# Kernel tuning notes

Hardware: AMD Instinct MI355X
Metric: run time of the kernel (lower is better)

Reference implementation:

```python
import math
import jax, jax.numpy as jnp
import numpy as np
from jax import lax

# Block_mamba(dim=192): x = x + Mamba(LN1(x)); x = x + EinFFT(LN2(x), H, W)
DIM = 192
D_STATE = 64
D_CONV = 4
EXPAND = 2
D_INNER = EXPAND * DIM          # 384
DT_RANK = math.ceil(DIM / 16)   # 12
NUM_BLOCKS = 4                  # EinFFT hardcoded
BLOCK_SIZE = DIM // NUM_BLOCKS  # 48
LAMBDA = 0.01                   # softshrink threshold


def setup_inputs() -> dict:
    key = jax.random.key(0)
    ks = jax.random.split(key, 20)
    B, N, C = 4, 1024, DIM
    s = 0.02
    x = jax.random.normal(ks[0], (B, N, C), jnp.float32)
    inp = {
        "x": x,
        "ln1_w": jnp.ones((C,), jnp.float32),
        "ln1_b": jnp.zeros((C,), jnp.float32),
        "in_proj_w": jax.random.normal(ks[1], (2 * D_INNER, C), jnp.float32) * s,
        "conv_w": jax.random.normal(ks[2], (D_INNER, 1, D_CONV), jnp.float32) * 0.1,
        "conv_b": jnp.zeros((D_INNER,), jnp.float32),
        "x_proj_w": jax.random.normal(ks[3], (DT_RANK + 2 * D_STATE, D_INNER), jnp.float32) * s,
        "dt_proj_w": jax.random.normal(ks[4], (D_INNER, DT_RANK), jnp.float32) * (DT_RANK ** -0.5),
        "dt_proj_b": jax.random.uniform(ks[5], (D_INNER,), jnp.float32, -4.0, -2.0),
        "A_log": jnp.log(jnp.broadcast_to(jnp.arange(1, D_STATE + 1, dtype=jnp.float32), (D_INNER, D_STATE))),
        "D": jnp.ones((D_INNER,), jnp.float32),
        "out_proj_w": jax.random.normal(ks[6], (C, D_INNER), jnp.float32) * s,
        "ln2_w": jnp.ones((C,), jnp.float32),
        "ln2_b": jnp.zeros((C,), jnp.float32),
        "cw1": jax.random.normal(ks[7], (2, NUM_BLOCKS, BLOCK_SIZE, BLOCK_SIZE), jnp.float32) * s,
        "cw2": jax.random.normal(ks[8], (2, NUM_BLOCKS, BLOCK_SIZE, BLOCK_SIZE), jnp.float32) * s,
        "cb1": jax.random.normal(ks[9], (2, NUM_BLOCKS, BLOCK_SIZE), jnp.float32) * s,
        "cb2": jax.random.normal(ks[10], (2, NUM_BLOCKS, BLOCK_SIZE), jnp.float32) * s,
        "H": 32,
        "W": 32,
    }
    return inp


def layer_norm(x, w, b, eps=1e-5):
    mu = jnp.mean(x, axis=-1, keepdims=True)
    var = jnp.var(x, axis=-1, keepdims=True)
    return (x - mu) * lax.rsqrt(var + eps) * w + b


def mamba(x, in_proj_w, conv_w, conv_b, x_proj_w, dt_proj_w, dt_proj_b, A_log, D):
    B, L, C = x.shape
    xz = jnp.einsum('blc,ec->ble', x, in_proj_w)          # [B,L,2*D_INNER]
    xm, z = jnp.split(xz, 2, axis=-1)                      # each [B,L,D_INNER]
    # causal depthwise conv1d (torch pads both sides then slices [:, :, :L])
    xc = lax.conv_general_dilated(
        xm.transpose(0, 2, 1), conv_w, (1,), [(D_CONV - 1, 0)],
        dimension_numbers=('NCH', 'OIH', 'NCH'), feature_group_count=D_INNER)
    xm = jax.nn.silu(xc + conv_b[None, :, None]).transpose(0, 2, 1)  # [B,L,D_INNER]
    dbc = jnp.einsum('bld,ed->ble', xm, x_proj_w)
    dt, Bm, Cm = jnp.split(dbc, [DT_RANK, DT_RANK + D_STATE], axis=-1)
    delta = jax.nn.softplus(jnp.einsum('blr,dr->bld', dt, dt_proj_w) + dt_proj_b)  # [B,L,D_INNER]
    A = -jnp.exp(A_log)                                    # [D_INNER, D_STATE]

    def step(h, inp):
        d_t, B_t, C_t, x_t = inp                           # [B,d],[B,n],[B,n],[B,d]
        dA = jnp.exp(d_t[:, :, None] * A)                  # [B,d,n]
        h = h * dA + (d_t * x_t)[:, :, None] * B_t[:, None, :]
        y = jnp.einsum('bdn,bn->bd', h, C_t)
        return h, y

    h0 = jnp.zeros((B, D_INNER, D_STATE), x.dtype)
    xs = (delta.transpose(1, 0, 2), Bm.transpose(1, 0, 2), Cm.transpose(1, 0, 2), xm.transpose(1, 0, 2))
    _, ys = lax.scan(step, h0, xs)                         # ys: [L,B,d]
    y = ys.transpose(1, 0, 2) + xm * D
    y = y * jax.nn.silu(z)
    return jnp.einsum('bld,cd->blc', y, out_proj_w_global[0])


# small trick to keep mamba signature tidy
out_proj_w_global = [None]


def einfft(x, cw1, cw2, cb1, cb2):
    B, N, C = x.shape
    xv = x.reshape(B, N, NUM_BLOCKS, BLOCK_SIZE)
    pad1 = (1 << math.ceil(math.log2(N))) - N
    pad2 = (1 << math.ceil(math.log2(NUM_BLOCKS))) - NUM_BLOCKS
    if pad1 or pad2:
        xv = jnp.pad(xv, ((0, 0), (0, pad1), (0, pad2), (0, 0)))
    X = jnp.fft.fft2(xv, axes=(1, 2), norm='ortho')
    mul = lambda t, w: jnp.einsum('Bnbd,bdk->Bnbk', t, w)
    r1 = jax.nn.relu(mul(X.real, cw1[0]) - mul(X.imag, cw1[1]) + cb1[0])
    i1 = jax.nn.relu(mul(X.real, cw1[1]) + mul(X.imag, cw1[0]) + cb1[1])
    r2 = mul(r1, cw2[0]) - mul(i1, cw2[1]) + cb2[0]
    i2 = mul(r1, cw2[1]) + mul(i1, cw2[0]) + cb2[1]
    ss = lambda v: jnp.where(v > LAMBDA, v - LAMBDA, jnp.where(v < -LAMBDA, v + LAMBDA, jnp.zeros((), v.dtype)))
    Z = ss(r2) + 1j * ss(i2)
    y = jnp.fft.ifft2(Z, axes=(1, 2), norm='ortho')[:, :N, :NUM_BLOCKS, :]
    return y.real.reshape(B, N, C)  # torch .to(real dtype) keeps real part


def reference(x, ln1_w, ln1_b, in_proj_w, conv_w, conv_b, x_proj_w, dt_proj_w, dt_proj_b,
              A_log, D, out_proj_w, ln2_w, ln2_b, cw1, cw2, cb1, cb2, H, W):
    out_proj_w_global[0] = out_proj_w
    x = x + mamba(layer_norm(x, ln1_w, ln1_b), in_proj_w, conv_w, conv_b,
                  x_proj_w, dt_proj_w, dt_proj_b, A_log, D)
    x = x + einfft(layer_norm(x, ln2_w, ln2_b), cw1, cw2, cb1, cb2)
    return x
```

## Files before the change

### kernel.cpp

```cpp
#include <hip/hip_runtime.h>
#include <math.h>

#define PI_F 3.14159265358979323846f

__device__ __forceinline__ float lane_bcast(float v, int l) {
  return __int_as_float(__builtin_amdgcn_readlane(__float_as_int(v), l));
}

__device__ __forceinline__ float wave_reduce_sum(float v) {
  v += __shfl_xor(v, 32, 64);
  v += __shfl_xor(v, 16, 64);
  v += __shfl_xor(v, 8, 64);
  v += __shfl_xor(v, 4, 64);
  v += __shfl_xor(v, 2, 64);
  v += __shfl_xor(v, 1, 64);
  return v;
}

__global__ __launch_bounds__(256) void ln_kernel(const float* __restrict__ x,
    const float* __restrict__ w, const float* __restrict__ b, float* __restrict__ o) {
  int row = blockIdx.x * 4 + (threadIdx.x >> 6);
  int lane = threadIdx.x & 63;
  const float* xr = x + (size_t)row * 192;
  float v0 = xr[lane], v1 = xr[lane + 64], v2 = xr[lane + 128];
  float s  = wave_reduce_sum(v0 + v1 + v2);
  float s2 = wave_reduce_sum(v0 * v0 + v1 * v1 + v2 * v2);
  float mu  = s * (1.f / 192.f);
  float var = s2 * (1.f / 192.f) - mu * mu;
  float rs  = rsqrtf(var + 1e-5f);
  float* orow = o + (size_t)row * 192;
  orow[lane]       = (v0 - mu) * rs * w[lane]       + b[lane];
  orow[lane + 64]  = (v1 - mu) * rs * w[lane + 64]  + b[lane + 64];
  orow[lane + 128] = (v2 - mu) * rs * w[lane + 128] + b[lane + 128];
}

__global__ __launch_bounds__(256) void ln2t_kernel(const float* __restrict__ x,
    const float* __restrict__ w, const float* __restrict__ b, float* __restrict__ xT) {
  __shared__ float xt[32][193];
  __shared__ float mu_s[32], rs_s[32];
  int blk = blockIdx.x;
  int Bi = blk >> 5;
  int t0 = (blk & 31) * 32;
  int tid = threadIdx.x;
  const float* xb = x + ((size_t)(Bi * 1024 + t0)) * 192;
  for (int i = tid; i < 32 * 192; i += 256) {
    xt[i / 192][i % 192] = xb[i];
  }
  __syncthreads();
  int row = tid >> 3, seg = tid & 7;
  float s = 0.f, s2 = 0.f;
  const float* xr = &xt[row][seg * 24];
#pragma unroll
  for (int k = 0; k < 24; ++k) { float v = xr[k]; s += v; s2 += v * v; }
  s  += __shfl_xor(s, 1, 64);  s  += __shfl_xor(s, 2, 64);  s  += __shfl_xor(s, 4, 64);
  s2 += __shfl_xor(s2, 1, 64); s2 += __shfl_xor(s2, 2, 64); s2 += __shfl_xor(s2, 4, 64);
  if (seg == 0) {
    float mu = s * (1.f / 192.f);
    float var = s2 * (1.f / 192.f) - mu * mu;
    mu_s[row] = mu;
    rs_s[row] = rsqrtf(var + 1e-5f);
  }
  __syncthreads();
  for (int i = tid; i < 32 * 192; i += 256) {
    int ch = i >> 5, r2 = i & 31;
    float v = (xt[r2][ch] - mu_s[r2]) * rs_s[r2] * w[ch] + b[ch];
    xT[((size_t)(Bi * 192 + ch)) * 1024 + t0 + r2] = v;
  }
}

__global__ __launch_bounds__(256) void gemm_tn(const float* __restrict__ A,
    const float* __restrict__ W, const float* __restrict__ res, float* __restrict__ C,
    int M, int N, int K) {
  __shared__ float As[2][32][68];
  __shared__ float Ws[2][32][68];
  int tid = threadIdx.x;
  int m0 = blockIdx.y * 64, n0 = blockIdx.x * 64;
  int tr = tid >> 4, tc = tid & 15;
  int sm  = tid >> 3;
  int skq = tid & 7;
  float4 aP[2], wP[2];
#pragma unroll
  for (int j = 0; j < 2; ++j) {
    int m = sm + j * 32;
    aP[j] = *(const float4*)(A + (size_t)(m0 + m) * K + skq * 4);
    int n = n0 + m;
    if (n < N) wP[j] = *(const float4*)(W + (size_t)n * K + skq * 4);
    else       wP[j] = make_float4(0.f, 0.f, 0.f, 0.f);
  }
#pragma unroll
  for (int j = 0; j < 2; ++j) {
    int m = sm + j * 32;
    As[0][skq * 4 + 0][m] = aP[j].x;
    As[0][skq * 4 + 1][m] = aP[j].y;
    As[0][skq * 4 + 2][m] = aP[j].z;
    As[0][skq * 4 + 3][m] = aP[j].w;
    Ws[0][skq * 4 + 0][m] = wP[j].x;
    Ws[0][skq * 4 + 1][m] = wP[j].y;
    Ws[0][skq * 4 + 2][m] = wP[j].z;
    Ws[0][skq * 4 + 3][m] = wP[j].w;
  }
  __syncthreads();
  float acc[4][4] = {{0.f}};
  int nk = K >> 5;
  for (int it = 0; it < nk; ++it) {
    int cur = it & 1, nxt = cur ^ 1;
    if (it + 1 < nk) {
      int kk = (it + 1) << 5;
#pragma unroll
      for (int j = 0; j < 2; ++j) {
        int m = sm + j * 32;
        aP[j] = *(const float4*)(A + (size_t)(m0 + m) * K + kk + skq * 4);
        int n = n0 + m;
        if (n < N) wP[j] = *(const float4*)(W + (size_t)n * K + kk + skq * 4);
        else       wP[j] = make_float4(0.f, 0.f, 0.f, 0.f);
      }
    }
#pragma unroll
    for (int k = 0; k < 32; ++k) {
      float4 a4 = *(const float4*)&As[cur][k][tr * 4];
      float4 w4 = *(const float4*)&Ws[cur][k][tc * 4];
      float a[4] = {a4.x, a4.y, a4.z, a4.w};
      float bb[4] = {w4.x, w4.y, w4.z, w4.w};
#pragma unroll
      for (int i = 0; i < 4; ++i)
#pragma unroll
        for (int j = 0; j < 4; ++j)
          acc[i][j] = fmaf(a[i], bb[j], acc[i][j]);
    }
    if (it + 1 < nk) {
#pragma unroll
      for (int j = 0; j < 2; ++j) {
        int m = sm + j * 32;
        As[nxt][skq * 4 + 0][m] = aP[j].x;
        As[nxt][skq * 4 + 1][m] = aP[j].y;
        As[nxt][skq * 4 + 2][m] = aP[j].z;
        As[nxt][skq * 4 + 3][m] = aP[j].w;
        Ws[nxt][skq * 4 + 0][m] = wP[j].x;
        Ws[nxt][skq * 4 + 1][m] = wP[j].y;
        Ws[nxt][skq * 4 + 2][m] = wP[j].z;
        Ws[nxt][skq * 4 + 3][m] = wP[j].w;
      }
      __syncthreads();
    }
  }
#pragma unroll
  for (int i = 0; i < 4; ++i) {
    int m = m0 + tr * 4 + i;
#pragma unroll
    for (int j = 0; j < 4; ++j) {
      int n = n0 + tc * 4 + j;
      if (n < N) {
        float v = acc[i][j];
        if (res) v += res[m * N + n];
        C[m * N + n] = v;
      }
    }
  }
}

__global__ __launch_bounds__(256) void gemm_tn32(const float* __restrict__ A,
    const float* __restrict__ W, const float* __restrict__ res, float* __restrict__ C,
    int M, int N, int K) {
  __shared__ float As[2][32][36];
  __shared__ float Ws[2][32][68];
  int tid = threadIdx.x;
  int m0 = blockIdx.y * 32, n0 = blockIdx.x * 64;
  int tr = tid >> 4, tc = tid & 15;
  int sm  = tid >> 3;
  int skq = tid & 7;
  float4 aP, wP[2];
  aP = *(const float4*)(A + (size_t)(m0 + sm) * K + skq * 4);
#pragma unroll
  for (int j = 0; j < 2; ++j) {
    int n = n0 + sm + j * 32;
    if (n < N) wP[j] = *(const float4*)(W + (size_t)n * K + skq * 4);
    else       wP[j] = make_float4(0.f, 0.f, 0.f, 0.f);
  }
  As[0][skq * 4 + 0][sm] = aP.x;
  As[0][skq * 4 + 1][sm] = aP.y;
  As[0][skq * 4 + 2][sm] = aP.z;
  As[0][skq * 4 + 3][sm] = aP.w;
#pragma unroll
  for (int j = 0; j < 2; ++j) {
    int n = sm + j * 32;
    Ws[0][skq * 4 + 0][n] = wP[j].x;
    Ws[0][skq * 4 + 1][n] = wP[j].y;
    Ws[0][skq * 4 + 2][n] = wP[j].z;
    Ws[0][skq * 4 + 3][n] = wP[j].w;
  }
  __syncthreads();
  float acc[2][4] = {{0.f}};
  int nk = K >> 5;
  for (int it = 0; it < nk; ++it) {
    int cur = it & 1, nxt = cur ^ 1;
    if (it + 1 < nk) {
      int kk = (it + 1) << 5;
      aP = *(const float4*)(A + (size_t)(m0 + sm) * K + kk + skq * 4);
#pragma unroll
      for (int j = 0; j < 2; ++j) {
        int n = n0 + sm + j * 32;
        if (n < N) wP[j] = *(const float4*)(W + (size_t)n * K + kk + skq * 4);
        else       wP[j] = make_float4(0.f, 0.f, 0.f, 0.f);
      }
    }
#pragma unroll
    for (int k = 0; k < 32; ++k) {
      float2 a2 = *(const float2*)&As[cur][k][tr * 2];
      float4 w4 = *(const float4*)&Ws[cur][k][tc * 4];
      float a[2] = {a2.x, a2.y};
      float bb[4] = {w4.x, w4.y, w4.z, w4.w};
#pragma unroll
      for (int i = 0; i < 2; ++i)
#pragma unroll
        for (int j = 0; j < 4; ++j)
          acc[i][j] = fmaf(a[i], bb[j], acc[i][j]);
    }
    if (it + 1 < nk) {
      As[nxt][skq * 4 + 0][sm] = aP.x;
      As[nxt][skq * 4 + 1][sm] = aP.y;
      As[nxt][skq * 4 + 2][sm] = aP.z;
      As[nxt][skq * 4 + 3][sm] = aP.w;
#pragma unroll
      for (int j = 0; j < 2; ++j) {
        int n = sm + j * 32;
        Ws[nxt][skq * 4 + 0][n] = wP[j].x;
        Ws[nxt][skq * 4 + 1][n] = wP[j].y;
        Ws[nxt][skq * 4 + 2][n] = wP[j].z;
        Ws[nxt][skq * 4 + 3][n] = wP[j].w;
      }
      __syncthreads();
    }
  }
#pragma unroll
  for (int i = 0; i < 2; ++i) {
    int m = m0 + tr * 2 + i;
#pragma unroll
    for (int j = 0; j < 4; ++j) {
      int n = n0 + tc * 4 + j;
      if (n < N) {
        float v = acc[i][j];
        if (res) v += res[m * N + n];
        C[m * N + n] = v;
      }
    }
  }
}

__global__ __launch_bounds__(256) void gemm_at32(const float* __restrict__ AT,
    const float* __restrict__ W, const float* __restrict__ res, float* __restrict__ C,
    int M, int N, int K) {
  __shared__ float As[2][32][36];
  __shared__ float Ws[2][32][68];
  int tid = threadIdx.x;
  int m0 = blockIdx.y * 32, n0 = blockIdx.x * 64;
  int bb = m0 >> 10;
  int t0 = m0 & 1023;
  const float* Ab = AT + ((size_t)bb * K) * 1024 + t0;
  int tr = tid >> 4, tc = tid & 15;
  int sm  = tid >> 3;
  int skq = tid & 7;
  float4 aP, wP[2];
  aP = *(const float4*)(Ab + (size_t)sm * 1024 + skq * 4);
#pragma unroll
  for (int j = 0; j < 2; ++j) {
    int n = n0 + sm + j * 32;
    if (n < N) wP[j] = *(const float4*)(W + (size_t)n * K + skq * 4);
    else       wP[j] = make_float4(0.f, 0.f, 0.f, 0.f);
  }
  *(float4*)&As[0][sm][skq * 4] = aP;
#pragma unroll
  for (int j = 0; j < 2; ++j) {
    int n = sm + j * 32;
    Ws[0][skq * 4 + 0][n] = wP[j].x;
    Ws[0][skq * 4 + 1][n] = wP[j].y;
    Ws[0][skq * 4 + 2][n] = wP[j].z;
    Ws[0][skq * 4 + 3][n] = wP[j].w;
  }
  __syncthreads();
  float acc[2][4] = {{0.f}};
  int nk = K >> 5;
  for (int it = 0; it < nk; ++it) {
    int cur = it & 1, nxt = cur ^ 1;
    if (it + 1 < nk) {
      int kk = (it + 1) << 5;
      aP = *(const float4*)(Ab + (size_t)(kk + sm) * 1024 + skq * 4);
#pragma unroll
      for (int j = 0; j < 2; ++j) {
        int n = n0 + sm + j * 32;
        if (n < N) wP[j] = *(const float4*)(W + (size_t)n * K + kk + skq * 4);
        else       wP[j] = make_float4(0.f, 0.f, 0.f, 0.f);
      }
    }
#pragma unroll
    for (int k = 0; k < 32; ++k) {
      float2 a2 = *(const float2*)&As[cur][k][tr * 2];
      float4 w4 = *(const float4*)&Ws[cur][k][tc * 4];
      float a[2] = {a2.x, a2.y};
      float bb4[4] = {w4.x, w4.y, w4.z, w4.w};
#pragma unroll
      for (int i = 0; i < 2; ++i)
#pragma unroll
        for (int j = 0; j < 4; ++j)
          acc[i][j] = fmaf(a[i], bb4[j], acc[i][j]);
    }
    if (it + 1 < nk) {
      *(float4*)&As[nxt][sm][skq * 4] = aP;
#pragma unroll
      for (int j = 0; j < 2; ++j) {
        int n = sm + j * 32;
        Ws[nxt][skq * 4 + 0][n] = wP[j].x;
        Ws[nxt][skq * 4 + 1][n] = wP[j].y;
        Ws[nxt][skq * 4 + 2][n] = wP[j].z;
        Ws[nxt][skq * 4 + 3][n] = wP[j].w;
      }
      __syncthreads();
    }
  }
#pragma unroll
  for (int i = 0; i < 2; ++i) {
    int m = m0 + tr * 2 + i;
#pragma unroll
    for (int j = 0; j < 4; ++j) {
      int n = n0 + tc * 4 + j;
      if (n < N) {
        float v = acc[i][j];
        if (res) v += res[m * N + n];
        C[m * N + n] = v;
      }
    }
  }
}

__global__ __launch_bounds__(256) void conv_silu(const float* __restrict__ xz,
    const float* __restrict__ cw, const float* __restrict__ cb, float* __restrict__ xc) {
  int e4 = blockIdx.x * 256 + threadIdx.x;
  if (e4 >= 4 * 1024 * 96) return;
  int d4 = e4 % 96;
  int t  = (e4 / 96) % 1024;
  int b  = e4 / (96 * 1024);
  int d = d4 * 4;
  const float* base = xz + (size_t)(b * 1024) * 768 + d;
  float4 acc = *(const float4*)(cb + d);
  const float4* cwv = (const float4*)(cw + d * 4);
  float4 c0 = cwv[0], c1 = cwv[1], c2 = cwv[2], c3 = cwv[3];
#pragma unroll
  for (int j = 0; j < 4; ++j) {
    int tt = t - 3 + j;
    if (tt >= 0) {
      float4 v = *(const float4*)(base + (size_t)tt * 768);
      float w0 = (&c0.x)[j], w1 = (&c1.x)[j], w2 = (&c2.x)[j], w3 = (&c3.x)[j];
      acc.x = fmaf(v.x, w0, acc.x);
      acc.y = fmaf(v.y, w1, acc.y);
      acc.z = fmaf(v.z, w2, acc.z);
      acc.w = fmaf(v.w, w3, acc.w);
    }
  }
  float4 o;
  o.x = acc.x / (1.f + __expf(-acc.x));
  o.y = acc.y / (1.f + __expf(-acc.y));
  o.z = acc.z / (1.f + __expf(-acc.z));
  o.w = acc.w / (1.f + __expf(-acc.w));
  *(float4*)(xc + ((size_t)(b * 1024 + t) * 384) + d) = o;
}

__global__ __launch_bounds__(256) void delta_trans(const float* __restrict__ dbc,
    const float* __restrict__ dtw, const float* __restrict__ dtb,
    const float* __restrict__ xc, float* __restrict__ dltT, float* __restrict__ duT) {
  __shared__ float dts[64][13];
  __shared__ float xt[64][65];
  int blk = blockIdx.x;
  int b  = blk / 96;
  int rem = blk % 96;
  int tt = rem / 6, dd = rem % 6;
  int t0 = tt * 64, d0 = dd * 64;
  int tid = threadIdx.x;
  for (int i = tid; i < 64 * 12; i += 256) {
    int tl = i / 12, r = i % 12;
    dts[tl][r] = dbc[((size_t)b * 1024 + t0 + tl) * 140 + r];
  }
  {
    int col = tid & 63, rg = tid >> 6;
#pragma unroll
    for (int j = 0; j < 16; ++j) {
      int row = j * 4 + rg;
      xt[row][col] = xc[((size_t)b * 1024 + t0 + row) * 384 + d0 + col];
    }
  }
  __syncthreads();
  int tl = tid & 63, grp = tid >> 6;
#pragma unroll
  for (int j = 0; j < 16; ++j) {
    int dl = grp * 16 + j;
    int d = d0 + dl;
    float s = dtb[d];
#pragma unroll
    for (int r = 0; r < 12; ++r) s += dts[tl][r] * dtw[d * 12 + r];
    float dlt = (s > 20.f) ? s : log1pf(__expf(s));
    size_t ob = ((size_t)b * 384 + d) * 1024 + t0 + tl;
    dltT[ob] = dlt;
    duT[ob]  = dlt * xt[tl][dl];
  }
}

__global__ __launch_bounds__(128) void scan_pc(const float* __restrict__ dltT,
    const float* __restrict__ duT, const float* __restrict__ dbc,
    const float* __restrict__ A_log, const float* __restrict__ xc,
    const float* __restrict__ xz, const float* __restrict__ Dvec,
    float* __restrict__ yT) {
  __shared__ float Bs[2][16][64];
  __shared__ float Cs[2][16][64];
  __shared__ float dvs[2][64], dus[2][64];
  __shared__ float xcs[2][16], zvs[2][16];
  __shared__ float tile[16][65];
  int bd = blockIdx.x;
  int b = bd / 384, d = bd % 384;
  int tid = threadIdx.x;
  int wv = tid >> 6;
  int lane = tid & 63;
  const float* dT = dltT + ((size_t)b * 384 + d) * 1024;
  const float* uT = duT  + ((size_t)b * 384 + d) * 1024;
  const float* Bbase = dbc + (size_t)(b * 1024) * 140 + 12;
  const float* xcp = xc + (size_t)(b * 1024) * 384 + d;
  const float* xzp = xz + (size_t)(b * 1024) * 768 + 384 + d;
  float* yp = yT + ((size_t)b * 384 + d) * 1024;

  float A = 0.f, ddv = 0.f;
  int tq = lane & 15, q = lane >> 4;
  if (wv == 1) {
#pragma unroll
    for (int i = 0; i < 16; ++i) {
      size_t ro = (size_t)i * 140 + lane;
      Bs[0][i][lane] = Bbase[ro];
      Cs[0][i][lane] = Bbase[ro + 64];
    }
    dvs[0][lane] = dT[lane];
    dus[0][lane] = uT[lane];
    if (lane < 16) {
      xcs[0][lane] = xcp[(size_t)lane * 384];
      zvs[0][lane] = xzp[(size_t)lane * 768];
    }
  } else {
    A = -__expf(A_log[d * 64 + lane]) * 1.44269504f;
    ddv = Dvec[d];
  }
  __syncthreads();

  float h = 0.f, dv64 = 0.f, du64 = 0.f;
  for (int g = 0; g < 64; ++g) {
    int cur = g & 1, nxt = cur ^ 1;
    if (wv == 1) {
      if (g < 63) {
        int ts1 = (g + 1) * 16;
#pragma unroll
        for (int i = 0; i < 16; ++i) {
          size_t ro = (size_t)(ts1 + i) * 140 + lane;
          Bs[nxt][i][lane] = Bbase[ro];
          Cs[nxt][i][lane] = Bbase[ro + 64];
        }
        if (lane < 16) {
          xcs[nxt][lane] = xcp[(size_t)(ts1 + lane) * 384];
          zvs[nxt][lane] = xzp[(size_t)(ts1 + lane) * 768];
        }
        if (((g + 1) & 3) == 0) {
          int sseg = (g + 1) >> 2;
          int sl = sseg & 1;
          dvs[sl][lane] = dT[sseg * 64 + lane];
          dus[sl][lane] = uT[sseg * 64 + lane];
        }
      }
    } else {
      if ((g & 3) == 0) {
        int sl = (g >> 2) & 1;
        dv64 = dvs[sl][lane];
        du64 = dus[sl][lane];
      }
      int ts = g * 16, tb = ts & 63;
      float Bv[16], Cv[16];
#pragma unroll
      for (int i = 0; i < 16; ++i) {
        Bv[i] = Bs[cur][i][lane];
        Cv[i] = Cs[cur][i][lane];
      }
      float xcv = 0.f, zv = 0.f;
      if (lane < 16) { xcv = xcs[cur][lane]; zv = zvs[cur][lane]; }
#pragma unroll
      for (int i = 0; i < 16; ++i) {
        float sdv = lane_bcast(dv64, tb + i);
        float sdu = lane_bcast(du64, tb + i);
        float a = exp2f(sdv * A);
        h = fmaf(h, a, sdu * Bv[i]);
        tile[i][lane] = h * Cv[i];
      }
      const float* trow = &tile[tq][q * 16];
      float s_ = 0.f;
#pragma unroll
      for (int i = 0; i < 16; ++i) s_ += trow[i];
      s_ += __shfl_xor(s_, 16, 64);
      s_ += __shfl_xor(s_, 32, 64);
      if (lane < 16) {
        float sg = zv / (1.f + __expf(-zv));
        yp[ts + lane] = (s_ + xcv * ddv) * sg;
      }
    }
    __syncthreads();
  }
}

__device__ __forceinline__ int rev4_10(int i) {
  unsigned r = __brev((unsigned)i) >> 22;
  return (int)(((r & 0x155u) << 1) | ((r >> 1) & 0x155u));
}

__device__ __forceinline__ void fft1024r4(float* __restrict__ re,
    float* __restrict__ im, const float* __restrict__ twc,
    const float* __restrict__ tws, int tid, float sgn) {
  for (int i = tid; i < 1024; i += 256) {
    int r = rev4_10(i);
    if (i < r) {
      float t = re[i]; re[i] = re[r]; re[r] = t;
      t = im[i]; im[i] = im[r]; im[r] = t;
    }
  }
  __syncthreads();
  {
    float4 ar = *(float4*)&re[tid * 4];
    float4 ai = *(float4*)&im[tid * 4];
    float apc_r = ar.x + ar.z, amc_r = ar.x - ar.z;
    float apc_i = ai.x + ai.z, amc_i = ai.x - ai.z;
    float bpd_r = ar.y + ar.w, bmd_r = ar.y - ar.w;
    float bpd_i = ai.y + ai.w, bmd_i = ai.y - ai.w;
    float4 yr, yi;
    yr.x = apc_r + bpd_r;        yi.x = apc_i + bpd_i;
    yr.z = apc_r - bpd_r;        yi.z = apc_i - bpd_i;
    yr.y = amc_r - sgn * bmd_i;  yi.y = amc_i + sgn * bmd_r;
    yr.w = amc_r + sgn * bmd_i;  yi.w = amc_i - sgn * bmd_r;
    *(float4*)&re[tid * 4] = yr;
    *(float4*)&im[tid * 4] = yi;
  }
  __syncthreads();
#pragma unroll
  for (int s = 1; s < 5; ++s) {
    int L = 1 << (2 * s);
    int tstep = 256 >> (2 * s);
    int j = tid & (L - 1);
    int base = ((tid >> (2 * s)) << (2 * s + 2)) + j;
    int i0 = base, i1 = base + L, i2 = base + 2 * L, i3 = base + 3 * L;
    int x1i = j * tstep;
    float w1c = twc[x1i],     w1s = tws[x1i];
    float w2c = twc[2 * x1i], w2s = tws[2 * x1i];
    float w3c = twc[3 * x1i], w3s = tws[3 * x1i];
    float ar_ = re[i0], ai_ = im[i0];
    float br_ = re[i1], bi_ = im[i1];
    float cr_ = re[i2], ci_ = im[i2];
    float dr_ = re[i3], di_ = im[i3];
    float tbr = br_ * w1c - bi_ * w1s, tbi = br_ * w1s + bi_ * w1c;
    float tcr = cr_ * w2c - ci_ * w2s, tci = cr_ * w2s + ci_ * w2c;
    float tdr = dr_ * w3c - di_ * w3s, tdi = dr_ * w3s + di_ * w3c;
    float apc_r = ar_ + tcr, amc_r = ar_ - tcr;
    float apc_i = ai_ + tci, amc_i = ai_ - tci;
    float bpd_r = tbr + tdr, bmd_r = tbr - tdr;
    float bpd_i = tbi + tdi, bmd_i = tbi - tdi;
    re[i0] = apc_r + bpd_r;       im[i0] = apc_i + bpd_i;
    re[i2] = apc_r - bpd_r;       im[i2] = apc_i - bpd_i;
    re[i1] = amc_r - sgn * bmd_i; im[i1] = amc_i + sgn * bmd_r;
    re[i3] = amc_r + sgn * bmd_i; im[i3] = amc_i - sgn * bmd_r;
    __syncthreads();
  }
}

__global__ __launch_bounds__(256) void fft_fwd(const float* __restrict__ x2T,
    float* __restrict__ Xre, float* __restrict__ Xim) {
  __shared__ float re[1024];
  __shared__ float im[1024];
  __shared__ float twc[768];
  __shared__ float tws[768];
  int blk = blockIdx.x;
  int c = blk & 3;
  int rest = blk >> 2;
  int d = rest % 48, Bi = rest / 48;
  int tid = threadIdx.x;
  for (int k = tid; k < 768; k += 256) {
    float sv, cv;
    __sincosf(-PI_F * (float)k * (1.f / 512.f), &sv, &cv);
    twc[k] = cv; tws[k] = sv;
  }
  const float* pb = x2T + ((size_t)(Bi * 192 + d)) * 1024;
  for (int n = tid; n < 1024; n += 256) {
    float v0 = pb[n];
    float v1 = pb[48 * 1024 + n];
    float v2 = pb[96 * 1024 + n];
    float v3 = pb[144 * 1024 + n];
    float rr, ii;
    if (c == 0)      { rr = v0 + v1 + v2 + v3; ii = 0.f; }
    else if (c == 1) { rr = v0 - v2;           ii = -(v1 - v3); }
    else if (c == 2) { rr = v0 - v1 + v2 - v3; ii = 0.f; }
    else             { rr = v0 - v2;           ii = (v1 - v3); }
    re[n] = rr; im[n] = ii;
  }
  __syncthreads();
  fft1024r4(re, im, twc, tws, tid, -1.0f);
  float* xo_r = Xre + ((size_t)((Bi * 4 + c) * 48 + d)) * 1024;
  float* xo_i = Xim + ((size_t)((Bi * 4 + c) * 48 + d)) * 1024;
  for (int k = tid; k < 1024; k += 256) {
    xo_r[k] = re[k] * (1.f / 64.f);
    xo_i[k] = im[k] * (1.f / 64.f);
  }
}

__global__ __launch_bounds__(256) void mix_fused(float* __restrict__ Xre,
    float* __restrict__ Xim, const float* __restrict__ cw1,
    const float* __restrict__ cw2, const float* __restrict__ cb1,
    const float* __restrict__ cb2) {
  __shared__ float r1s[4][48][4];
  __shared__ float i1s[4][48][4];
  int w = threadIdx.x >> 6;
  int j = threadIdx.x & 63;
  int rg = blockIdx.x * 4 + w;
  int kq = rg & 255;
  int b  = (rg >> 8) & 3;
  int Bi = rg >> 10;
  int k0 = kq * 4;
  size_t xbase = ((size_t)((Bi * 4 + b) * 48)) * 1024 + k0;
  if (j < 48) {
    const float* wr = cw1 + b * 2304;
    const float* wi = cw1 + 9216 + b * 2304;
    float b1r = cb1[b * 48 + j], b1i = cb1[192 + b * 48 + j];
    float ar[4] = {b1r, b1r, b1r, b1r};
    float ai[4] = {b1i, b1i, b1i, b1i};
#pragma unroll 8
    for (int dd = 0; dd < 48; ++dd) {
      float4 xr = *(const float4*)(Xre + xbase + (size_t)dd * 1024);
      float4 xi = *(const float4*)(Xim + xbase + (size_t)dd * 1024);
      float wrv = wr[dd * 48 + j], wiv = wi[dd * 48 + j];
      ar[0] = fmaf(xr.x, wrv, ar[0]); ar[0] = fmaf(-xi.x, wiv, ar[0]);
      ai[0] = fmaf(xr.x, wiv, ai[0]); ai[0] = fmaf(xi.x, wrv, ai[0]);
      ar[1] = fmaf(xr.y, wrv, ar[1]); ar[1] = fmaf(-xi.y, wiv, ar[1]);
      ai[1] = fmaf(xr.y, wiv, ai[1]); ai[1] = fmaf(xi.y, wrv, ai[1]);
      ar[2] = fmaf(xr.z, wrv, ar[2]); ar[2] = fmaf(-xi.z, wiv, ar[2]);
      ai[2] = fmaf(xr.z, wiv, ai[2]); ai[2] = fmaf(xi.z, wrv, ai[2]);
      ar[3] = fmaf(xr.w, wrv, ar[3]); ar[3] = fmaf(-xi.w, wiv, ar[3]);
      ai[3] = fmaf(xr.w, wiv, ai[3]); ai[3] = fmaf(xi.w, wrv, ai[3]);
    }
    float4 r1v, i1v;
    r1v.x = fmaxf(ar[0], 0.f); r1v.y = fmaxf(ar[1], 0.f);
    r1v.z = fmaxf(ar[2], 0.f); r1v.w = fmaxf(ar[3], 0.f);
    i1v.x = fmaxf(ai[0], 0.f); i1v.y = fmaxf(ai[1], 0.f);
    i1v.z = fmaxf(ai[2], 0.f); i1v.w = fmaxf(ai[3], 0.f);
    *(float4*)&r1s[w][j][0] = r1v;
    *(float4*)&i1s[w][j][0] = i1v;
    const float* wr2 = cw2 + b * 2304;
    const float* wi2 = cw2 + 9216 + b * 2304;
    float b2r = cb2[b * 48 + j], b2i = cb2[192 + b * 48 + j];
    float a2r[4] = {b2r, b2r, b2r, b2r};
    float a2i[4] = {b2i, b2i, b2i, b2i};
#pragma unroll 8
    for (int dd = 0; dd < 48; ++dd) {
      float4 rv = *(const float4*)&r1s[w][dd][0];
      float4 iv = *(const float4*)&i1s[w][dd][0];
      float wrv = wr2[dd * 48 + j], wiv = wi2[dd * 48 + j];
      a2r[0] = fmaf(rv.x, wrv, a2r[0]); a2r[0] = fmaf(-iv.x, wiv, a2r[0]);
      a2i[0] = fmaf(rv.x, wiv, a2i[0]); a2i[0] = fmaf(iv.x, wrv, a2i[0]);
      a2r[1] = fmaf(rv.y, wrv, a2r[1]); a2r[1] = fmaf(-iv.y, wiv, a2r[1]);
      a2i[1] = fmaf(rv.y, wiv, a2i[1]); a2i[1] = fmaf(iv.y, wrv, a2i[1]);
      a2r[2] = fmaf(rv.z, wrv, a2r[2]); a2r[2] = fmaf(-iv.z, wiv, a2r[2]);
      a2i[2] = fmaf(rv.z, wiv, a2i[2]); a2i[2] = fmaf(iv.z, wrv, a2i[2]);
      a2r[3] = fmaf(rv.w, wrv, a2r[3]); a2r[3] = fmaf(-iv.w, wiv, a2r[3]);
      a2i[3] = fmaf(rv.w, wiv, a2i[3]); a2i[3] = fmaf(iv.w, wrv, a2i[3]);
    }
    float4 zr, zi;
#pragma unroll
    for (int r = 0; r < 4; ++r) {
      float vr = a2r[r], vi = a2i[r];
      (&zr.x)[r] = (vr > 0.01f) ? vr - 0.01f : ((vr < -0.01f) ? vr + 0.01f : 0.f);
      (&zi.x)[r] = (vi > 0.01f) ? vi - 0.01f : ((vi < -0.01f) ? vi + 0.01f : 0.f);
    }
    size_t obase = ((size_t)((Bi * 4 + b) * 48 + j)) * 1024 + k0;
    *(float4*)(Xre + obase) = zr;
    *(float4*)(Xim + obase) = zi;
  }
}

__global__ __launch_bounds__(256) void fft_inv(const float* __restrict__ Zre,
    const float* __restrict__ Zim, const float* __restrict__ x1, float* __restrict__ out) {
  __shared__ float re[1024];
  __shared__ float im[1024];
  __shared__ float twc[768];
  __shared__ float tws[768];
  int blk = blockIdx.x;
  int c = blk & 3;
  int rest = blk >> 2;
  int d = rest % 48, Bi = rest / 48;
  int tid = threadIdx.x;
  for (int k = tid; k < 768; k += 256) {
    float sv, cv;
    __sincosf(PI_F * (float)k * (1.f / 512.f), &sv, &cv);
    twc[k] = cv; tws[k] = sv;
  }
  const float* zr0 = Zre + ((size_t)((Bi * 4) * 48 + d)) * 1024;
  const float* zi0 = Zim + ((size_t)((Bi * 4) * 48 + d)) * 1024;
  const int cs = 48 * 1024;
  for (int k = tid; k < 1024; k += 256) {
    float r0 = zr0[k], r1v = zr0[cs + k], r2 = zr0[2 * cs + k], r3 = zr0[3 * cs + k];
    float i0 = zi0[k], i1v = zi0[cs + k], i2 = zi0[2 * cs + k], i3 = zi0[3 * cs + k];
    float rr, ii;
    if (c == 0)      { rr = r0 + r1v + r2 + r3;  ii = i0 + i1v + i2 + i3; }
    else if (c == 1) { rr = r0 - i1v - r2 + i3;  ii = i0 + r1v - i2 - r3; }
    else if (c == 2) { rr = r0 - r1v + r2 - r3;  ii = i0 - i1v + i2 - i3; }
    else             { rr = r0 + i1v - r2 - i3;  ii = i0 - r1v - i2 + r3; }
    re[k] = rr; im[k] = ii;
  }
  __syncthreads();
  fft1024r4(re, im, twc, tws, tid, 1.0f);
  for (int n = tid; n < 1024; n += 256) {
    size_t o = (size_t)(Bi * 1024 + n) * 192 + c * 48 + d;
    out[o] = x1[o] + re[n] * (1.f / 64.f);
  }
}

extern "C" void kernel_launch(void* const* d_in, const int* in_sizes, int n_in,
                              void* d_out, int out_size, void* d_ws, size_t ws_size,
                              hipStream_t stream) {
  const float* x         = (const float*)d_in[0];
  const float* ln1_w     = (const float*)d_in[1];
  const float* ln1_b     = (const float*)d_in[2];
  const float* in_proj_w = (const float*)d_in[3];
  const float* conv_w    = (const float*)d_in[4];
  const float* conv_b    = (const float*)d_in[5];
  const float* x_proj_w  = (const float*)d_in[6];
  const float* dt_proj_w = (const float*)d_in[7];
  const float* dt_proj_b = (const float*)d_in[8];
  const float* A_log     = (const float*)d_in[9];
  const float* Dvec      = (const float*)d_in[10];
  const float* out_proj_w= (const float*)d_in[11];
  const float* ln2_w     = (const float*)d_in[12];
  const float* ln2_b     = (const float*)d_in[13];
  const float* cw1       = (const float*)d_in[14];
  const float* cw2       = (const float*)d_in[15];
  const float* cb1       = (const float*)d_in[16];
  const float* cb2       = (const float*)d_in[17];
  float* out = (float*)d_out;
  float* ws  = (float*)d_ws;

  float* xz   = ws;
  float* xc   = xz  + 3145728;
  float* dbc  = xc  + 1572864;
  float* dltT = dbc + 573440;
  float* yvT  = dltT + 1572864;
  float* xln  = yvT + 1572864;
  float* x2T  = xln + 786432;
  float* Xre  = x2T + 786432;
  float* Xim  = Xre + 786432;
  float* duT = Xre;
  float* x1 = xln;

  ln_kernel<<<1024, 256, 0, stream>>>(x, ln1_w, ln1_b, xln);
  gemm_tn<<<dim3(12, 64), 256, 0, stream>>>(xln, in_proj_w, nullptr, xz, 4096, 768, 192);
  conv_silu<<<1536, 256, 0, stream>>>(xz, conv_w, conv_b, xc);
  gemm_tn32<<<dim3(3, 128), 256, 0, stream>>>(xc, x_proj_w, nullptr, dbc, 4096, 140, 384);
  delta_trans<<<384, 256, 0, stream>>>(dbc, dt_proj_w, dt_proj_b, xc, dltT, duT);
  scan_pc<<<1536, 128, 0, stream>>>(dltT, duT, dbc, A_log, xc, xz, Dvec, yvT);
  gemm_at32<<<dim3(3, 128), 256, 0, stream>>>(yvT, out_proj_w, x, x1, 4096, 192, 384);
  ln2t_kernel<<<128, 256, 0, stream>>>(x1, ln2_w, ln2_b, x2T);
  fft_fwd<<<768, 256, 0, stream>>>(x2T, Xre, Xim);
  mix_fused<<<1024, 256, 0, stream>>>(Xre, Xim, cw1, cw2, cb1, cb2);
  fft_inv<<<768, 256, 0, stream>>>(Xre, Xim, x1, out);
}
```

Before: 350.5 us.

## Replace producer/consumer scan with single-wave scan using async global-to-LDS loads

The selective-scan kernel drops its dedicated loader wave and barriers. A single 64-lane wave now prefetches the next B/C chunk with global_load_lds (direct global-to-LDS DMA) and register-prefetches xc/z/delta, then waits on vmcnt at the end of each step. This removes the __syncthreads and the extra wave's LDS store traffic, but halves the threads per block and relies on the explicit waitcnt for ordering. LDS reuse of the tile between iterations within one wave needs no barrier.

```diff
diff --git a/kernel.cpp b/kernel.cpp
--- a/kernel.cpp
+++ b/kernel.cpp
@@ -402,107 +402,104 @@
   }
 }
 
-__global__ __launch_bounds__(128) void scan_pc(const float* __restrict__ dltT,
+__global__ __launch_bounds__(64, 1) void scan_glds(const float* __restrict__ dltT,
     const float* __restrict__ duT, const float* __restrict__ dbc,
     const float* __restrict__ A_log, const float* __restrict__ xc,
     const float* __restrict__ xz, const float* __restrict__ Dvec,
     float* __restrict__ yT) {
   __shared__ float Bs[2][16][64];
   __shared__ float Cs[2][16][64];
-  __shared__ float dvs[2][64], dus[2][64];
-  __shared__ float xcs[2][16], zvs[2][16];
   __shared__ float tile[16][65];
   int bd = blockIdx.x;
   int b = bd / 384, d = bd % 384;
-  int tid = threadIdx.x;
-  int wv = tid >> 6;
-  int lane = tid & 63;
+  int lane = threadIdx.x;
+  float A = -__expf(A_log[d * 64 + lane]) * 1.44269504f;
   const float* dT = dltT + ((size_t)b * 384 + d) * 1024;
   const float* uT = duT  + ((size_t)b * 384 + d) * 1024;
-  const float* Bbase = dbc + (size_t)(b * 1024) * 140 + 12;
+  const float* Bp = dbc + (size_t)(b * 1024) * 140 + 12 + lane;
+  const float* Cp = Bp + 64;
+  float ddv = Dvec[d];
+  float* yp = yT + ((size_t)b * 384 + d) * 1024;
   const float* xcp = xc + (size_t)(b * 1024) * 384 + d;
   const float* xzp = xz + (size_t)(b * 1024) * 768 + 384 + d;
-  float* yp = yT + ((size_t)b * 384 + d) * 1024;
-
-  float A = 0.f, ddv = 0.f;
   int tq = lane & 15, q = lane >> 4;
-  if (wv == 1) {
-#pragma unroll
-    for (int i = 0; i < 16; ++i) {
-      size_t ro = (size_t)i * 140 + lane;
-      Bs[0][i][lane] = Bbase[ro];
-      Cs[0][i][lane] = Bbase[ro + 64];
-    }
-    dvs[0][lane] = dT[lane];
-    dus[0][lane] = uT[lane];
-    if (lane < 16) {
-      xcs[0][lane] = xcp[(size_t)lane * 384];
-      zvs[0][lane] = xzp[(size_t)lane * 768];
-    }
-  } else {
-    A = -__expf(A_log[d * 64 + lane]) * 1.44269504f;
-    ddv = Dvec[d];
-  }
-  __syncthreads();
-
-  float h = 0.f, dv64 = 0.f, du64 = 0.f;
+
+#pragma unroll
+  for (int i = 0; i < 16; ++i) {
+    __builtin_amdgcn_global_load_lds(Bp + i * 140, &Bs[0][i][0], 4, 0, 0);
+    __builtin_amdgcn_global_load_lds(Cp + i * 140, &Cs[0][i][0], 4, 0, 0);
+  }
+  float h = 0.f;
+  float dv64 = dT[lane];
+  float du64 = uT[lane];
+  float xcv = 0.f, zv = 0.f;
+  if (lane < 16) {
+    xcv = xcp[(size_t)lane * 384];
+    zv  = xzp[(size_t)lane * 768];
+  }
+  asm volatile("s_waitcnt vmcnt(0)" ::: "memory");
+  __builtin_amdgcn_sched_barrier(0);
+
   for (int g = 0; g < 64; ++g) {
     int cur = g & 1, nxt = cur ^ 1;
-    if (wv == 1) {
-      if (g < 63) {
-        int ts1 = (g + 1) * 16;
+    if (g + 1 < 64) {
+      const float* Bg = Bp + (size_t)(g + 1) * (16 * 140);
+      const float* Cg = Cp + (size_t)(g + 1) * (16 * 140);
+      if (nxt) {
 #pragma unroll
         for (int i = 0; i < 16; ++i) {
-          size_t ro = (size_t)(ts1 + i) * 140 + lane;
-          Bs[nxt][i][lane] = Bbase[ro];
-          Cs[nxt][i][lane] = Bbase[ro + 64];
+          __builtin_amdgcn_global_load_lds(Bg + i * 140, &Bs[1][i][0], 4, 0, 0);
+          __builtin_amdgcn_global_load_lds(Cg + i * 140, &Cs[1][i][0], 4, 0, 0);
         }
-        if (lane < 16) {
-          xcs[nxt][lane] = xcp[(size_t)(ts1 + lane) * 384];
-          zvs[nxt][lane] = xzp[(size_t)(ts1 + lane) * 768];
+      } else {
+#pragma unroll
+        for (int i = 0; i < 16; ++i) {
+          __builtin_amdgcn_global_load_lds(Bg + i * 140, &Bs[0][i][0], 4, 0, 0);
+          __builtin_amdgcn_global_load_lds(Cg + i * 140, &Cs[0][i][0], 4, 0, 0);
         }
-        if (((g + 1) & 3) == 0) {
-          int sseg = (g + 1) >> 2;
-          int sl = sseg & 1;
-          dvs[sl][lane] = dT[sseg * 64 + lane];
-          dus[sl][lane] = uT[sseg * 64 + lane];
-        }
-      }
-    } else {
-      if ((g & 3) == 0) {
-        int sl = (g >> 2) & 1;
-        dv64 = dvs[sl][lane];
-        du64 = dus[sl][lane];
-      }
-      int ts = g * 16, tb = ts & 63;
-      float Bv[16], Cv[16];
-#pragma unroll
-      for (int i = 0; i < 16; ++i) {
-        Bv[i] = Bs[cur][i][lane];
-        Cv[i] = Cs[cur][i][lane];
-      }
-      float xcv = 0.f, zv = 0.f;
-      if (lane < 16) { xcv = xcs[cur][lane]; zv = zvs[cur][lane]; }
-#pragma unroll
-      for (int i = 0; i < 16; ++i) {
-        float sdv = lane_bcast(dv64, tb + i);
-        float sdu = lane_bcast(du64, tb + i);
-        float a = exp2f(sdv * A);
-        h = fmaf(h, a, sdu * Bv[i]);
-        tile[i][lane] = h * Cv[i];
-      }
-      const float* trow = &tile[tq][q * 16];
-      float s_ = 0.f;
-#pragma unroll
-      for (int i = 0; i < 16; ++i) s_ += trow[i];
-      s_ += __shfl_xor(s_, 16, 64);
-      s_ += __shfl_xor(s_, 32, 64);
+      }
+    }
+    float xcvN = 0.f, zvN = 0.f, dvN = dv64, duN = du64;
+    if (g + 1 < 64) {
+      int ts1 = (g + 1) * 16;
       if (lane < 16) {
-        float sg = zv / (1.f + __expf(-zv));
-        yp[ts + lane] = (s_ + xcv * ddv) * sg;
-      }
-    }
-    __syncthreads();
+        xcvN = xcp[(size_t)(ts1 + lane) * 384];
+        zvN  = xzp[(size_t)(ts1 + lane) * 768];
+      }
+      if (((g + 1) & 3) == 0) {
+        int sg = (g + 1) >> 2;
+        dvN = dT[sg * 64 + lane];
+        duN = uT[sg * 64 + lane];
+      }
+    }
+    int tb = (g & 3) * 16;
+    float Bv[16], Cv[16];
+#pragma unroll
+    for (int i = 0; i < 16; ++i) {
+      Bv[i] = Bs[cur][i][lane];
+      Cv[i] = Cs[cur][i][lane];
+    }
+#pragma unroll
+    for (int i = 0; i < 16; ++i) {
+      float sdv = lane_bcast(dv64, tb + i);
+      float sdu = lane_bcast(du64, tb + i);
+      float a = exp2f(sdv * A);
+      h = fmaf(h, a, sdu * Bv[i]);
+      tile[i][lane] = h * Cv[i];
+    }
+    const float* trow = &tile[tq][q * 16];
+    float s_ = 0.f;
+#pragma unroll
+    for (int i = 0; i < 16; ++i) s_ += trow[i];
+    s_ += __shfl_xor(s_, 16, 64);
+    s_ += __shfl_xor(s_, 32, 64);
+    if (lane < 16) {
+      float sg2 = zv / (1.f + __expf(-zv));
+      yp[g * 16 + lane] = (s_ + xcv * ddv) * sg2;
+    }
+    xcv = xcvN; zv = zvN; dv64 = dvN; du64 = duN;
+    asm volatile("s_waitcnt vmcnt(0)" ::: "memory");
+    __builtin_amdgcn_sched_barrier(0);
   }
 }
 
@@ -758,7 +755,7 @@
   conv_silu<<<1536, 256, 0, stream>>>(xz, conv_w, conv_b, xc);
   gemm_tn32<<<dim3(3, 128), 256, 0, stream>>>(xc, x_proj_w, nullptr, dbc, 4096, 140, 384);
   delta_trans<<<384, 256, 0, stream>>>(dbc, dt_proj_w, dt_proj_b, xc, dltT, duT);
-  scan_pc<<<1536, 128, 0, stream>>>(dltT, duT, dbc, A_log, xc, xz, Dvec, yvT);
+  scan_glds<<<1536, 64, 0, stream>>>(dltT, duT, dbc, A_log, xc, xz, Dvec, yvT);
   gemm_at32<<<dim3(3, 128), 256, 0, stream>>>(yvT, out_proj_w, x, x1, 4096, 192, 384);
   ln2t_kernel<<<128, 256, 0, stream>>>(x1, ln2_w, ln2_b, x2T);
   fft_fwd<<<768, 256, 0, stream>>>(x2T, Xre, Xim);
```

Measured after the change: 373.5 us. 6.6% more time.
